# Kernel tuning notes

Hardware: AMD Instinct MI355X
Metric: run time of the kernel (lower is better)

Reference implementation:

```python
import jax, jax.numpy as jnp
import numpy as np

LS, BS, N_HID, N_PART, T, D_IN, M = 2, 16, 256, 512, 16, 64, 1
MID = N_PART // 2


def setup_inputs() -> dict:
    key = jax.random.key(0)
    ks = jax.random.split(key, 12)
    s = 0.1
    inp = {}
    inp["x"] = jax.random.normal(ks[0], (BS, T, D_IN), jnp.float32)
    inp["y"] = jax.random.normal(ks[1], (BS,), jnp.float32)
    inp["particles"] = jax.random.normal(ks[2], (LS, BS, N_HID, N_PART), jnp.float32)
    inp["weights"] = jnp.full((BS, N_PART), 1.0 / N_PART, jnp.float32)
    inp["q"] = jnp.asarray(1.0, jnp.float32)
    inp["e"] = jnp.asarray(0.1, jnp.float32)
    inp["r"] = jnp.asarray(0.5, jnp.float32)
    inp["Wih0"] = jax.random.normal(ks[3], (4 * N_HID, D_IN), jnp.float32) * s
    inp["Whh0"] = jax.random.normal(ks[4], (4 * N_HID, N_HID), jnp.float32) * s
    inp["b0"] = jnp.zeros((4 * N_HID,), jnp.float32)
    inp["Wih1"] = jax.random.normal(ks[5], (4 * N_HID, N_HID), jnp.float32) * s
    inp["Whh1"] = jax.random.normal(ks[6], (4 * N_HID, N_HID), jnp.float32) * s
    inp["b1"] = jnp.zeros((4 * N_HID,), jnp.float32)
    inp["Wh"] = jax.random.normal(ks[7], (M, N_HID), jnp.float32) * s
    inp["bh"] = jnp.zeros((M,), jnp.float32)
    inp["eps_h"] = jax.random.normal(ks[8], (MID, LS, BS, N_HID), jnp.float32)
    inp["eps_c"] = jax.random.normal(ks[9], (MID, LS, BS, N_HID), jnp.float32)
    u = jax.random.uniform(ks[10], (BS, 2, MID), jnp.float32, minval=1e-6, maxval=1.0)
    inp["gumbel"] = -jnp.log(-jnp.log(u))  # Gumbel noise for multinomial resampling
    return inp


def _lstm(x, h0, c0, Wih0, Whh0, b0, Wih1, Whh1, b1, q2, e2, eps_h, eps_c):
    # x: [bs,T,d]; h0,c0: [ls,bs,n]. Two-layer LSTM, noise added to final states.
    xs = jnp.swapaxes(x, 0, 1)  # [T,bs,d]

    def make_step(Wih, Whh, b):
        def step(carry, xt):
            h, c = carry
            g = xt @ Wih.T + h @ Whh.T + b
            i, f, gg, o = jnp.split(g, 4, axis=-1)
            c2 = jax.nn.sigmoid(f) * c + jax.nn.sigmoid(i) * jnp.tanh(gg)
            h2 = jax.nn.sigmoid(o) * jnp.tanh(c2)
            return (h2, c2), h2
        return step

    (hA, cA), out0 = jax.lax.scan(make_step(Wih0, Whh0, b0), (h0[0], c0[0]), xs)
    (hB, cB), out1 = jax.lax.scan(make_step(Wih1, Whh1, b1), (h0[1], c0[1]), out0)
    hT = jnp.stack([hA, hB]) + jnp.sqrt(q2) * eps_h
    cT = jnp.stack([cA, cB]) + jnp.sqrt(e2) * eps_c
    return jnp.swapaxes(out1, 0, 1), hT, cT


def _obs(u_last, Wh, bh):  # u_last: [bs,n,N] -> [bs,m,N]
    return jnp.einsum('mn,bnN->bmN', Wh, u_last) + bh[None, :, None]


def _estimate(Y, w, r):
    # Y: [bs,m,N], w: [bs,N]
    w_sum = jnp.sum(w, -1)
    W_mu = jnp.einsum('bmN,bN->bm', Y, w) / w_sum[:, None]
    cen = Y - W_mu[:, :, None]
    cov = jnp.einsum('bmN,bkN->bmk', cen, cen) / (Y.shape[-1] - 1)
    cov = cov + jnp.eye(Y.shape[1], dtype=Y.dtype) * (r * r)
    return W_mu, cov


def _inv_logdet(sig):
    m = sig.shape[-1]
    sig = sig + 1e-6 * jnp.eye(m, dtype=sig.dtype)
    L = jnp.linalg.cholesky(sig)
    inv_sig = jnp.linalg.inv(jnp.swapaxes(L, -2, -1)) @ jnp.linalg.inv(L)
    logdet = jnp.linalg.slogdet(sig)[1]
    return inv_sig, logdet


def reference(x, y, particles, weights, q, e, r, Wih0, Whh0, b0, Wih1, Whh1, b1, Wh, bh, eps_h, eps_c, gumbel):
    q2, e2 = q * q, e * e  # noise is squared before the transition (TransitionF)
    # ---- forecast_PF: particle i is h, particle i+MID is c ----
    h_parts = jnp.moveaxis(particles[..., :MID], -1, 0)  # [MID,ls,bs,n]
    c_parts = jnp.moveaxis(particles[..., MID:], -1, 0)
    step_fn = jax.vmap(lambda h0, c0, eh, ec: _lstm(x, h0, c0, Wih0, Whh0, b0, Wih1, Whh1, b1, q2, e2, eh, ec)[1:])
    hN, cN = step_fn(h_parts, c_parts, eps_h, eps_c)
    pr = jnp.moveaxis(jnp.concatenate([hN, cN], 0), 0, -1)  # [ls,bs,n,N]

    # ---- torch_PF weight update ----
    w = jnp.log(weights)
    Y = _obs(pr[-1], Wh, bh)  # [bs,m,N]
    W_mu_e, sig_e = _estimate(Y, w, r)  # NOTE: original passes LOG weights here (faithful)
    inv_sig, logdet = _inv_logdet(sig_e)
    w_sum = jnp.sum(w, -1)
    Wmu2 = Y * w[:, None, :] / w_sum[:, None, None]  # elementwise, as in w_likelihood
    innov = y[:, None, None] - Wmu2  # [bs,m,N]
    quad = jnp.einsum('bmN,bmk,bkN->bN', innov, inv_sig, innov)
    new_w = w + (-0.5 * logdet[:, None] - 0.5 * quad)
    # original: new_w -= log(sum(exp(new_w))) where python-sum reduces dim 0 -> [N]
    new_w = new_w - jnp.log(jnp.sum(jnp.exp(new_w), axis=0))[None, :]
    new_w = jnp.exp(new_w)

    # ---- per-batch, per-half soft resampling when neff < N/4 ----
    def resample_half(p, wh, g):  # p [ls,n,MID], wh [MID], g [MID]
        neff = 1.0 / jnp.sum(wh * wh)
        do = neff < (N_PART / 4.0)
        soft = 0.5 * wh + 0.5 / MID
        idx = jnp.argsort(-(jnp.log(soft) + g))  # weighted sample w/o replacement (Gumbel top-k)
        p_r = p[:, :, idx]
        lw = jnp.log(wh / soft)
        w_r = jnp.exp(lw - jax.nn.logsumexp(lw))
        return jnp.where(do, p_r, p), jnp.where(do, w_r, wh)

    def per_batch(p_b, w_b, g_b):  # p_b [ls,n,N], w_b [N], g_b [2,MID]
        p1, w1 = resample_half(p_b[:, :, :MID], w_b[:MID], g_b[0])
        p2, w2 = resample_half(p_b[:, :, MID:], w_b[MID:], g_b[1])
        return jnp.concatenate([p1, p2], -1), jnp.concatenate([w1, w2], 0)

    pf, wf = jax.vmap(per_batch, in_axes=(1, 0, 0), out_axes=(1, 0))(pr, new_w, gumbel)

    # ---- train=True branch: estimate / likelihood / NIS on filtered ensemble ----
    Yf = _obs(pf[-1], Wh, bh)
    W_mu, sig = _estimate(Yf, wf, r)
    inv_s, ld = _inv_logdet(sig)
    inn = y[:, None] - W_mu  # [bs,m]
    qf = jnp.einsum('bm,bmk,bk->b', inn, inv_s, inn)
    l = jnp.sum(-0.5 * ld - 0.5 * qf)
    nis = jnp.mean(qf)
    return W_mu, sig, pf, wf, l, nis
```

## Files before the change

### kernel.cpp

```cpp
#include <hip/hip_runtime.h>
#include <hip/hip_bf16.h>
#include <math.h>

#define LSN 2
#define BSN 16
#define NH 256
#define NP 512
#define MIDP 256
#define TTN 16
#define DIN 64
#define NCH 4096
#define GW 1024
#define PRS 268

typedef _Float16 f16;
typedef _Float16 f16x8 __attribute__((ext_vector_type(8)));
typedef float f32x4 __attribute__((ext_vector_type(4)));

__device__ __forceinline__ float fsig(float x){ return 1.0f/(1.0f+expf(-x)); }

__device__ __forceinline__ float brsum(float v, float* red){
  int tid = threadIdx.x;
  red[tid]=v; __syncthreads();
  for (int s=128; s>0; s>>=1){ if (tid<s) red[tid]+=red[tid+s]; __syncthreads(); }
  float r = red[0]; __syncthreads(); return r;
}

__device__ __forceinline__ int gsrow(int jp){
  return ((jp>>5)&3)*NH + (jp>>7)*32 + (jp&31);
}

__global__ void k_prep_w0(const float* __restrict__ Whh0, f16* __restrict__ W0i){
  int jp = blockIdx.x; int srow = gsrow(jp);
  W0i[(size_t)jp*NH + threadIdx.x] = (f16)Whh0[(size_t)srow*NH + threadIdx.x];
}
__global__ void k_prep_w1(const float* __restrict__ Wih1, const float* __restrict__ Whh1, f16* __restrict__ W1c){
  int jp = blockIdx.x; int srow = gsrow(jp);
  for (int p=0;p<2;++p){
    int k = p*256 + threadIdx.x;
    float v = (k < 256) ? Wih1[(size_t)srow*NH + k] : Whh1[(size_t)srow*NH + (k-256)];
    W1c[(size_t)jp*512 + k] = (f16)v;
  }
}
__global__ void k_prep_b1(const float* __restrict__ b1, float* __restrict__ b1i){
  int jp = blockIdx.x*256 + threadIdx.x;
  b1i[jp] = b1[gsrow(jp)];
}
__global__ void k_prep_xw0(const float* __restrict__ x, const float* __restrict__ Wih0,
                           const float* __restrict__ b0, float* __restrict__ xW0){
  int row = blockIdx.x;
  __shared__ float xr[DIN];
  if (threadIdx.x < DIN) xr[threadIdx.x] = x[(size_t)row*DIN + threadIdx.x];
  __syncthreads();
  int n = threadIdx.x;
  for (int q=0;q<4;++q){
    int wrow = q*NH + n;
    float acc = b0[wrow];
    #pragma unroll 8
    for (int d=0; d<DIN; ++d) acc += xr[d] * Wih0[(size_t)wrow*DIN + d];
    int jhat = (n>>5)*128 + q*32 + (n&31);
    xW0[(size_t)row*GW + jhat] = acc;
  }
}

__global__ __launch_bounds__(256) void k_init(const float* __restrict__ part,
                f16* __restrict__ h0, f16* __restrict__ h1,
                float* __restrict__ c0, float* __restrict__ c1){
  __shared__ float lh[64][65];
  __shared__ float lcv[64][65];
  int l = blockIdx.z, b = blockIdx.y;
  int i0 = (blockIdx.x >> 2)*64, n0 = (blockIdx.x & 3)*64;
  int tid = threadIdx.x;
  #pragma unroll
  for (int rep=0; rep<16; ++rep){
    int nn = rep*4 + (tid>>6);
    int ii = tid & 63;
    size_t rowb = ((size_t)(l*BSN + b)*NH + n0 + nn)*NP;
    lh[nn][ii]  = part[rowb + i0 + ii];
    lcv[nn][ii] = part[rowb + MIDP + i0 + ii];
  }
  __syncthreads();
  f16* h = l ? h1 : h0;
  float* c = l ? c1 : c0;
  #pragma unroll
  for (int rep=0; rep<16; ++rep){
    int ii = rep*4 + (tid>>6);
    int nn = tid & 63;
    size_t chain = (size_t)b*256 + i0 + ii;
    h[chain*NH + n0 + nn] = (f16)lh[nn][ii];
    c[chain*NH + n0 + nn] = lcv[nn][ii];
  }
}

struct StepCfg {
  const f16* A1; const f16* A2;
  float* C; f16* Hout;
  int layer; int t; int is_last;
};

__global__ __launch_bounds__(256) void k_step2(
    StepCfg cfgA, StepCfg cfgB,
    const f16* __restrict__ W0i, const f16* __restrict__ W1c,
    const float* __restrict__ xw0, const float* __restrict__ b1i,
    float* __restrict__ pr, const float* __restrict__ eps_h, const float* __restrict__ eps_c,
    const float* __restrict__ qp, const float* __restrict__ ep)
{
  __shared__ __align__(16) char smem[36864];
  f16* Asm = (f16*)smem;
  f16* Bsm = Asm + 128*72;

  const StepCfg cfg = blockIdx.z ? cfgB : cfgA;
  const int layer  = cfg.layer;
  const int Kt     = layer ? 512 : 256;
  const int nslice = layer ? 8 : 4;
  const f16* W     = layer ? W1c : W0i;

  const int tid = threadIdx.x;
  const int lane = tid & 63, wid = tid >> 6;
  const int lr = lane >> 4, lc = lane & 15;
  const int wm = wid * 32;
  const int m0 = blockIdx.x * 128;
  const int y  = blockIdx.y;
  const int bb = blockIdx.x >> 1;

  float cold[2][2][4];
  #pragma unroll
  for (int mi=0; mi<2; ++mi)
    #pragma unroll
    for (int mh=0; mh<2; ++mh)
      #pragma unroll
      for (int r=0; r<4; ++r)
        cold[mi][mh][r] = cfg.C[(size_t)(m0 + wm + mi*16 + lr*4 + r)*NH + y*32 + mh*16 + lc];

  f32x4 acc[2][8];
  #pragma unroll
  for (int mi=0;mi<2;++mi)
    #pragma unroll
    for (int ni=0;ni<8;++ni) acc[mi][ni] = (f32x4){0.f,0.f,0.f,0.f};

  const int srow = tid >> 1, sseg = (tid & 1)*32;
  for (int ks=0; ks<nslice; ++ks){
    __syncthreads();
    const f16* Ab; int ka;
    if (layer==1 && ks>=4){ Ab = cfg.A2; ka = (ks-4)*64; } else { Ab = cfg.A1; ka = ks*64; }
    {
      const float4* src = (const float4*)(Ab + (size_t)(m0+srow)*NH + ka + sseg);
      float4* dst = (float4*)(Asm + srow*72 + sseg);
      dst[0]=src[0]; dst[1]=src[1]; dst[2]=src[2]; dst[3]=src[3];
      const float4* srcB = (const float4*)(W + (size_t)(y*128+srow)*Kt + ks*64 + sseg);
      float4* dstB = (float4*)(Bsm + srow*72 + sseg);
      dstB[0]=srcB[0]; dstB[1]=srcB[1]; dstB[2]=srcB[2]; dstB[3]=srcB[3];
    }
    __syncthreads();
    #pragma unroll
    for (int k2=0;k2<2;++k2){
      const int koff = k2*32 + lr*8;
      f16x8 a0 = *(const f16x8*)(Asm + (wm +  0 + lc)*72 + koff);
      f16x8 a1 = *(const f16x8*)(Asm + (wm + 16 + lc)*72 + koff);
      f16x8 b[8];
      #pragma unroll
      for (int ni=0;ni<8;++ni) b[ni] = *(const f16x8*)(Bsm + (ni*16 + lc)*72 + koff);
      #pragma unroll
      for (int ni=0;ni<8;++ni){
        acc[0][ni] = __builtin_amdgcn_mfma_f32_16x16x32_f16(a0, b[ni], acc[0][ni], 0,0,0);
        acc[1][ni] = __builtin_amdgcn_mfma_f32_16x16x32_f16(a1, b[ni], acc[1][ni], 0,0,0);
      }
    }
  }

  float addv[4][2];
  {
    const float* ar = (layer==0) ? (xw0 + (size_t)(bb*TTN + cfg.t)*GW + y*128)
                                 : (b1i + y*128);
    #pragma unroll
    for (int q=0;q<4;++q)
      #pragma unroll
      for (int mh=0;mh<2;++mh)
        addv[q][mh] = ar[q*32 + mh*16 + lc];
  }

  float sq=0.f, se=0.f;
  float* prstage = (float*)smem;
  if (cfg.is_last){
    sq = sqrtf(qp[0]*qp[0]); se = sqrtf(ep[0]*ep[0]);
    __syncthreads();
  }

  #pragma unroll
  for (int mi=0;mi<2;++mi)
   #pragma unroll
   for (int mh=0;mh<2;++mh)
    #pragma unroll
    for (int r=0;r<4;++r){
      float gi = acc[mi][mh+0][r] + addv[0][mh];
      float gf = acc[mi][mh+2][r] + addv[1][mh];
      float gg = acc[mi][mh+4][r] + addv[2][mh];
      float go = acc[mi][mh+6][r] + addv[3][mh];
      float c2 = fsig(gf)*cold[mi][mh][r] + fsig(gi)*tanhf(gg);
      float h2 = fsig(go)*tanhf(c2);
      int ml = wm + mi*16 + lr*4 + r;
      int chain = m0 + ml;
      int nglob = y*32 + mh*16 + lc;
      cfg.Hout[(size_t)chain*NH + nglob] = (f16)h2;
      if (!cfg.is_last){
        cfg.C[(size_t)chain*NH + nglob] = c2;
      } else {
        int ip = (blockIdx.x & 1)*128 + ml;
        size_t eidx = ((size_t)(ip*LSN + layer)*BSN + bb)*NH + nglob;
        int nl = mh*16 + lc;
        prstage[nl*PRS + ml]       = h2 + sq*eps_h[eidx];
        prstage[nl*PRS + 128 + ml] = c2 + se*eps_c[eidx];
      }
    }

  if (cfg.is_last){
    __syncthreads();
    #pragma unroll
    for (int s=0;s<8;++s){
      int u = s*256 + tid;
      int nl = u >> 6, within = u & 63;
      int half = within >> 5, q4 = within & 31;
      size_t rowp = (size_t)(layer*BSN + bb)*NH + y*32 + nl;
      float4 v = *(const float4*)(prstage + nl*PRS + half*128 + q4*4);
      *(float4*)(pr + rowp*NP + half*MIDP + (blockIdx.x & 1)*128 + q4*4) = v;
    }
  }
}

__global__ void k_obs(const float* __restrict__ pr, const float* __restrict__ Wh,
                      const float* __restrict__ bh, float* __restrict__ Y){
  int b = blockIdx.x; int N = blockIdx.y*256 + threadIdx.x;
  float acc = bh[0];
  for (int n=0;n<NH;++n) acc += Wh[n] * pr[((size_t)(BSN + b)*NH + n)*NP + N];
  Y[(size_t)b*NP + N] = acc;
}

__global__ void k_stats1(const float* __restrict__ Y, const float* __restrict__ wts,
                         const float* __restrict__ yv, const float* __restrict__ rp,
                         float* __restrict__ pre){
  int b = blockIdx.x, tid = threadIdx.x;
  __shared__ float red[256];
  float lw0 = logf(wts[b*NP+tid]),     lw1 = logf(wts[b*NP+256+tid]);
  float y0  = Y[b*NP+tid],             y1  = Y[b*NP+256+tid];
  float SW = brsum(lw0+lw1, red);
  float SY = brsum(y0*lw0 + y1*lw1, red);
  float mu = SY/SW;
  float c0=y0-mu, c1=y1-mu;
  float SC = brsum(c0*c0+c1*c1, red);
  float sig = SC/511.0f + rp[0]*rp[0];
  float a = sig+1e-6f, inv = 1.0f/a, ld = logf(a);
  float yb = yv[b];
  float i0 = yb - y0*lw0/SW;
  float i1 = yb - y1*lw1/SW;
  pre[b*NP+tid]     = lw0 - 0.5f*ld - 0.5f*inv*i0*i0;
  pre[b*NP+256+tid] = lw1 - 0.5f*ld - 0.5f*inv*i1*i1;
}

__global__ void k_colsoftmax(const float* __restrict__ pre, float* __restrict__ neww){
  int N = blockIdx.x*256 + threadIdx.x;
  float s=0.f;
  for(int b=0;b<BSN;b++) s += expf(pre[b*NP+N]);
  float ls = logf(s);
  for(int b=0;b<BSN;b++) neww[b*NP+N] = expf(pre[b*NP+N] - ls);
}

__global__ void k_resample(const float* __restrict__ neww, const float* __restrict__ gum,
                           float* __restrict__ wf, int* __restrict__ idxb, int* __restrict__ dofl,
                           float* __restrict__ out){
  int b = blockIdx.x >> 1, hf = blockIdx.x & 1, j = threadIdx.x;
  __shared__ float red[256]; __shared__ float key[256];
  float wh = neww[b*NP + hf*256 + j];
  red[j] = wh*wh; __syncthreads();
  for (int s=128;s>0;s>>=1){ if(j<s) red[j]+=red[j+s]; __syncthreads(); }
  float s2 = red[0]; __syncthreads();
  int doit = (1.0f/s2) < (float)(NP)/4.0f;
  float soft = 0.5f*wh + (0.5f/(float)MIDP);
  float kk = logf(soft) + gum[(b*2+hf)*256 + j];
  key[j] = kk; __syncthreads();
  int rank = 0;
  for (int m=0;m<256;++m){ float km = key[m]; rank += (km > kk) || (km == kk && m < j); }
  idxb[(b*2+hf)*256 + rank] = j;
  float lw = logf(wh/soft);
  red[j] = lw; __syncthreads();
  for (int s=128;s>0;s>>=1){ if(j<s) red[j] = fmaxf(red[j],red[j+s]); __syncthreads(); }
  float mx = red[0]; __syncthreads();
  red[j] = expf(lw-mx); __syncthreads();
  for (int s=128;s>0;s>>=1){ if(j<s) red[j]+=red[j+s]; __syncthreads(); }
  float lse = mx + logf(red[0]);
  float wr = expf(lw - lse);
  float wv = doit ? wr : wh;
  wf[b*NP + hf*256 + j] = wv;
  out[4194336 + b*NP + hf*256 + j] = wv;
  if (j==0) dofl[b*2+hf] = doit;
}

__global__ void k_pfg(const float* __restrict__ pr, const int* __restrict__ idxb,
                      const int* __restrict__ dofl, float* __restrict__ out){
  size_t row = blockIdx.x;
  int b = (blockIdx.x >> 8) & 15;
  const float* src = pr + row*NP;
  for (int hf=0; hf<2; ++hf){
    int loc = threadIdx.x;
    int N = hf*256 + loc;
    int dcol = dofl[b*2+hf] ? hf*256 + idxb[(b*2+hf)*256 + loc] : N;
    out[32 + row*NP + N] = src[dcol];
  }
}

__global__ void k_yf(const float* __restrict__ Y, const int* __restrict__ idxb,
                     const int* __restrict__ dofl, float* __restrict__ Yf){
  int b = blockIdx.x; int N = threadIdx.x; int hf = N >> 8; int loc = N & 255;
  int dcol = dofl[b*2+hf] ? hf*256 + idxb[(b*2+hf)*256 + loc] : N;
  Yf[b*NP+N] = Y[b*NP+dcol];
}

__global__ void k_final_est(const float* __restrict__ Yf, const float* __restrict__ wf,
                            const float* __restrict__ yv, const float* __restrict__ rp,
                            float* __restrict__ qf, float* __restrict__ ldb,
                            float* __restrict__ out){
  int b = blockIdx.x, tid = threadIdx.x;
  __shared__ float red[256];
  float w0 = wf[b*NP+tid], w1 = wf[b*NP+256+tid];
  float y0 = Yf[b*NP+tid], y1 = Yf[b*NP+256+tid];
  float SW = brsum(w0+w1, red);
  float SY = brsum(y0*w0+y1*w1, red);
  float mu = SY/SW;
  float c0=y0-mu, c1=y1-mu;
  float SC = brsum(c0*c0+c1*c1, red);
  float sig = SC/511.0f + rp[0]*rp[0];
  if (tid==0){
    float a = sig + 1e-6f; float inv = 1.0f/a; float ld = logf(a);
    float inn = yv[b]-mu; float q = inn*inn*inv;
    qf[b]=q; ldb[b]=ld;
    out[b]      = mu;
    out[16 + b] = sig;
  }
}

__global__ void k_final_scalar(const float* __restrict__ qf, const float* __restrict__ ldb,
                               float* __restrict__ out){
  if (threadIdx.x==0){
    float l=0.f, nq=0.f;
    for(int b=0;b<BSN;b++){ l += -0.5f*ldb[b]-0.5f*qf[b]; nq += qf[b]; }
    out[4202528] = l;
    out[4202529] = nq/16.0f;
  }
}

extern "C" void kernel_launch(void* const* d_in, const int* in_sizes, int n_in,
                              void* d_out, int out_size, void* d_ws, size_t ws_size,
                              hipStream_t stream) {
  const float* x      = (const float*)d_in[0];
  const float* yv     = (const float*)d_in[1];
  const float* part   = (const float*)d_in[2];
  const float* wts    = (const float*)d_in[3];
  const float* qp     = (const float*)d_in[4];
  const float* ep     = (const float*)d_in[5];
  const float* rp     = (const float*)d_in[6];
  const float* Wih0   = (const float*)d_in[7];
  const float* Whh0   = (const float*)d_in[8];
  const float* b0     = (const float*)d_in[9];
  const float* Wih1   = (const float*)d_in[10];
  const float* Whh1   = (const float*)d_in[11];
  const float* b1     = (const float*)d_in[12];
  const float* Wh     = (const float*)d_in[13];
  const float* bh     = (const float*)d_in[14];
  const float* eps_h  = (const float*)d_in[15];
  const float* eps_c  = (const float*)d_in[16];
  const float* gum    = (const float*)d_in[17];
  float* out = (float*)d_out;

  char* p = (char*)d_ws;
  f16*   W0i  = (f16*)p;  p += (size_t)GW*NH*2;
  f16*   W1c  = (f16*)p;  p += (size_t)GW*512*2;
  float* b1i  = (float*)p; p += (size_t)GW*4;
  float* xW0  = (float*)p; p += (size_t)256*GW*4;
  f16*   h0A  = (f16*)p;  p += (size_t)NCH*NH*2;
  f16*   h0B  = (f16*)p;  p += (size_t)NCH*NH*2;
  f16*   h1A  = (f16*)p;  p += (size_t)NCH*NH*2;
  f16*   h1B  = (f16*)p;  p += (size_t)NCH*NH*2;
  float* c0   = (float*)p; p += (size_t)NCH*NH*4;
  float* c1   = (float*)p; p += (size_t)NCH*NH*4;
  float* pr   = (float*)p; p += (size_t)LSN*BSN*NH*NP*4;
  float* Yb   = (float*)p; p += 32768;
  float* pre  = (float*)p; p += 32768;
  float* neww = (float*)p; p += 32768;
  float* wf   = (float*)p; p += 32768;
  float* Yf   = (float*)p; p += 32768;
  int*   idxb = (int*)p;   p += 32768;
  int*   dofl = (int*)p;   p += 128;
  float* qf   = (float*)p; p += 64;
  float* ldb  = (float*)p; p += 64;

  k_prep_w0 <<<1024, 256, 0, stream>>>(Whh0, W0i);
  k_prep_w1 <<<1024, 256, 0, stream>>>(Wih1, Whh1, W1c);
  k_prep_b1 <<<4, 256, 0, stream>>>(b1, b1i);
  k_prep_xw0<<<256, 256, 0, stream>>>(x, Wih0, b0, xW0);
  k_init    <<<dim3(16,16,2), 256, 0, stream>>>(part, h0A, h1A, c0, c1);

  {
    StepCfg s0{h0A, nullptr, c0, h0B, 0, 0, 0};
    k_step2<<<dim3(32,8,1), 256, 0, stream>>>(s0, s0, W0i, W1c, xW0, b1i,
        pr, eps_h, eps_c, qp, ep);
  }
  f16 *h0cur=h0B, *h0nxt=h0A, *h1cur=h1A, *h1nxt=h1B;
  for (int t=0; t<15; ++t){
    StepCfg ca{h0cur, nullptr, c0, h0nxt, 0, t+1, (t+1==15) ? 1 : 0};
    StepCfg cb{h0cur, h1cur,   c1, h1nxt, 1, t,   0};
    k_step2<<<dim3(32,8,2), 256, 0, stream>>>(ca, cb, W0i, W1c, xW0, b1i,
        pr, eps_h, eps_c, qp, ep);
    f16* tmp = h0cur; h0cur = h0nxt; h0nxt = tmp;
    tmp = h1cur; h1cur = h1nxt; h1nxt = tmp;
  }
  {
    StepCfg fin{h0cur, h1cur, c1, h1nxt, 1, 15, 1};
    k_step2<<<dim3(32,8,1), 256, 0, stream>>>(fin, fin, W0i, W1c, xW0, b1i,
        pr, eps_h, eps_c, qp, ep);
  }

  k_obs       <<<dim3(16,2), 256, 0, stream>>>(pr, Wh, bh, Yb);
  k_stats1    <<<16, 256, 0, stream>>>(Yb, wts, yv, rp, pre);
  k_colsoftmax<<<2, 256, 0, stream>>>(pre, neww);
  k_resample  <<<32, 256, 0, stream>>>(neww, gum, wf, idxb, dofl, out);
  k_pfg       <<<8192, 256, 0, stream>>>(pr, idxb, dofl, out);
  k_yf        <<<16, 512, 0, stream>>>(Yb, idxb, dofl, Yf);
  k_final_est <<<16, 256, 0, stream>>>(Yf, wf, yv, rp, qf, ldb, out);
  k_final_scalar<<<1, 64, 0, stream>>>(qf, ldb, out);
}
```

Baseline: 432.6 us.

## Double-buffer LSTM step tiles, fuse prep/obs/stats/yf kernels, coarsen gather

The LSTM step kernel now prefetches the next K-slice into registers while the MFMAs run on the current slice. It uses two LDS buffers, so only one barrier is needed per slice. The three weight-prep kernels are merged into one, the observation and stats kernels are fused into a single 512-thread block per batch, and the Yf gather moves into the resample kernel. The particle gather kernel now runs 128 blocks, each copying 64 rows with a shared column map. Doubling LDS lowers possible occupancy, and the much smaller gather grid may underuse memory bandwidth.

```diff
diff --git a/kernel.cpp b/kernel.cpp
--- a/kernel.cpp
+++ b/kernel.cpp
@@ -12,6 +12,7 @@
 #define NCH 4096
 #define GW 1024
 #define PRS 268
+#define BUFSZ 36864
 
 typedef _Float16 f16;
 typedef _Float16 f16x8 __attribute__((ext_vector_type(8)));
@@ -19,6 +20,12 @@
 
 __device__ __forceinline__ float fsig(float x){ return 1.0f/(1.0f+expf(-x)); }
 
+__device__ __forceinline__ float brsum512(float v, float* red){
+  int tid = threadIdx.x;
+  red[tid]=v; __syncthreads();
+  for (int s=256; s>0; s>>=1){ if (tid<s) red[tid]+=red[tid+s]; __syncthreads(); }
+  float r = red[0]; __syncthreads(); return r;
+}
 __device__ __forceinline__ float brsum(float v, float* red){
   int tid = threadIdx.x;
   red[tid]=v; __syncthreads();
@@ -30,21 +37,14 @@
   return ((jp>>5)&3)*NH + (jp>>7)*32 + (jp&31);
 }
 
-__global__ void k_prep_w0(const float* __restrict__ Whh0, f16* __restrict__ W0i){
-  int jp = blockIdx.x; int srow = gsrow(jp);
-  W0i[(size_t)jp*NH + threadIdx.x] = (f16)Whh0[(size_t)srow*NH + threadIdx.x];
-}
-__global__ void k_prep_w1(const float* __restrict__ Wih1, const float* __restrict__ Whh1, f16* __restrict__ W1c){
-  int jp = blockIdx.x; int srow = gsrow(jp);
-  for (int p=0;p<2;++p){
-    int k = p*256 + threadIdx.x;
-    float v = (k < 256) ? Wih1[(size_t)srow*NH + k] : Whh1[(size_t)srow*NH + (k-256)];
-    W1c[(size_t)jp*512 + k] = (f16)v;
-  }
-}
-__global__ void k_prep_b1(const float* __restrict__ b1, float* __restrict__ b1i){
-  int jp = blockIdx.x*256 + threadIdx.x;
-  b1i[jp] = b1[gsrow(jp)];
+__global__ void k_prep_w(const float* __restrict__ Whh0, const float* __restrict__ Wih1,
+                         const float* __restrict__ Whh1, const float* __restrict__ b1,
+                         f16* __restrict__ W0i, f16* __restrict__ W1c, float* __restrict__ b1i){
+  int jp = blockIdx.x; int srow = gsrow(jp); int t = threadIdx.x;
+  W0i[(size_t)jp*NH + t]        = (f16)Whh0[(size_t)srow*NH + t];
+  W1c[(size_t)jp*512 + t]       = (f16)Wih1[(size_t)srow*NH + t];
+  W1c[(size_t)jp*512 + 256 + t] = (f16)Whh1[(size_t)srow*NH + t];
+  if (t==0) b1i[jp] = b1[srow];
 }
 __global__ void k_prep_xw0(const float* __restrict__ x, const float* __restrict__ Wih0,
                            const float* __restrict__ b0, float* __restrict__ xW0){
@@ -105,9 +105,7 @@
     float* __restrict__ pr, const float* __restrict__ eps_h, const float* __restrict__ eps_c,
     const float* __restrict__ qp, const float* __restrict__ ep)
 {
-  __shared__ __align__(16) char smem[36864];
-  f16* Asm = (f16*)smem;
-  f16* Bsm = Asm + 128*72;
+  __shared__ __align__(16) char smem[2*BUFSZ];
 
   const StepCfg cfg = blockIdx.z ? cfgB : cfgA;
   const int layer  = cfg.layer;
@@ -139,33 +137,49 @@
     for (int ni=0;ni<8;++ni) acc[mi][ni] = (f32x4){0.f,0.f,0.f,0.f};
 
   const int srow = tid >> 1, sseg = (tid & 1)*32;
-  for (int ks=0; ks<nslice; ++ks){
-    __syncthreads();
+
+  float4 ra0,ra1,ra2,ra3, rb0,rb1,rb2,rb3;
+  auto loadslice = [&](int ks){
     const f16* Ab; int ka;
     if (layer==1 && ks>=4){ Ab = cfg.A2; ka = (ks-4)*64; } else { Ab = cfg.A1; ka = ks*64; }
-    {
-      const float4* src = (const float4*)(Ab + (size_t)(m0+srow)*NH + ka + sseg);
-      float4* dst = (float4*)(Asm + srow*72 + sseg);
-      dst[0]=src[0]; dst[1]=src[1]; dst[2]=src[2]; dst[3]=src[3];
-      const float4* srcB = (const float4*)(W + (size_t)(y*128+srow)*Kt + ks*64 + sseg);
-      float4* dstB = (float4*)(Bsm + srow*72 + sseg);
-      dstB[0]=srcB[0]; dstB[1]=srcB[1]; dstB[2]=srcB[2]; dstB[3]=srcB[3];
-    }
-    __syncthreads();
+    const float4* sa = (const float4*)(Ab + (size_t)(m0+srow)*NH + ka + sseg);
+    const float4* sb = (const float4*)(W + (size_t)(y*128+srow)*Kt + (size_t)ks*64 + sseg);
+    ra0=sa[0]; ra1=sa[1]; ra2=sa[2]; ra3=sa[3];
+    rb0=sb[0]; rb1=sb[1]; rb2=sb[2]; rb3=sb[3];
+  };
+  auto writeslice = [&](int buf){
+    f16* base = (f16*)(smem + buf*BUFSZ);
+    float4* da = (float4*)(base + srow*72 + sseg);
+    da[0]=ra0; da[1]=ra1; da[2]=ra2; da[3]=ra3;
+    float4* db = (float4*)(base + 128*72 + srow*72 + sseg);
+    db[0]=rb0; db[1]=rb1; db[2]=rb2; db[3]=rb3;
+  };
+
+  loadslice(0);
+  writeslice(0);
+  __syncthreads();
+  for (int ks=0; ks<nslice; ++ks){
+    const int cur = ks & 1;
+    const bool more = (ks+1) < nslice;
+    if (more) loadslice(ks+1);
+    const f16* bufA = (const f16*)(smem + cur*BUFSZ);
+    const f16* bufB = bufA + 128*72;
     #pragma unroll
     for (int k2=0;k2<2;++k2){
       const int koff = k2*32 + lr*8;
-      f16x8 a0 = *(const f16x8*)(Asm + (wm +  0 + lc)*72 + koff);
-      f16x8 a1 = *(const f16x8*)(Asm + (wm + 16 + lc)*72 + koff);
+      f16x8 a0 = *(const f16x8*)(bufA + (wm +  0 + lc)*72 + koff);
+      f16x8 a1 = *(const f16x8*)(bufA + (wm + 16 + lc)*72 + koff);
       f16x8 b[8];
       #pragma unroll
-      for (int ni=0;ni<8;++ni) b[ni] = *(const f16x8*)(Bsm + (ni*16 + lc)*72 + koff);
+      for (int ni=0;ni<8;++ni) b[ni] = *(const f16x8*)(bufB + (ni*16 + lc)*72 + koff);
       #pragma unroll
       for (int ni=0;ni<8;++ni){
         acc[0][ni] = __builtin_amdgcn_mfma_f32_16x16x32_f16(a0, b[ni], acc[0][ni], 0,0,0);
         acc[1][ni] = __builtin_amdgcn_mfma_f32_16x16x32_f16(a1, b[ni], acc[1][ni], 0,0,0);
       }
     }
+    if (more) writeslice(cur ^ 1);
+    __syncthreads();
   }
 
   float addv[4][2];
@@ -183,7 +197,6 @@
   float* prstage = (float*)smem;
   if (cfg.is_last){
     sq = sqrtf(qp[0]*qp[0]); se = sqrtf(ep[0]*ep[0]);
-    __syncthreads();
   }
 
   #pragma unroll
@@ -227,33 +240,25 @@
   }
 }
 
-__global__ void k_obs(const float* __restrict__ pr, const float* __restrict__ Wh,
-                      const float* __restrict__ bh, float* __restrict__ Y){
-  int b = blockIdx.x; int N = blockIdx.y*256 + threadIdx.x;
+__global__ void k_obs_stats(const float* __restrict__ pr, const float* __restrict__ Wh,
+                            const float* __restrict__ bh, const float* __restrict__ wts,
+                            const float* __restrict__ yv, const float* __restrict__ rp,
+                            float* __restrict__ Y, float* __restrict__ pre){
+  int b = blockIdx.x; int N = threadIdx.x;
+  __shared__ float red[512];
   float acc = bh[0];
   for (int n=0;n<NH;++n) acc += Wh[n] * pr[((size_t)(BSN + b)*NH + n)*NP + N];
   Y[(size_t)b*NP + N] = acc;
-}
-
-__global__ void k_stats1(const float* __restrict__ Y, const float* __restrict__ wts,
-                         const float* __restrict__ yv, const float* __restrict__ rp,
-                         float* __restrict__ pre){
-  int b = blockIdx.x, tid = threadIdx.x;
-  __shared__ float red[256];
-  float lw0 = logf(wts[b*NP+tid]),     lw1 = logf(wts[b*NP+256+tid]);
-  float y0  = Y[b*NP+tid],             y1  = Y[b*NP+256+tid];
-  float SW = brsum(lw0+lw1, red);
-  float SY = brsum(y0*lw0 + y1*lw1, red);
+  float lw = logf(wts[b*NP+N]);
+  float SW = brsum512(lw, red);
+  float SY = brsum512(acc*lw, red);
   float mu = SY/SW;
-  float c0=y0-mu, c1=y1-mu;
-  float SC = brsum(c0*c0+c1*c1, red);
+  float cen = acc-mu;
+  float SC = brsum512(cen*cen, red);
   float sig = SC/511.0f + rp[0]*rp[0];
   float a = sig+1e-6f, inv = 1.0f/a, ld = logf(a);
-  float yb = yv[b];
-  float i0 = yb - y0*lw0/SW;
-  float i1 = yb - y1*lw1/SW;
-  pre[b*NP+tid]     = lw0 - 0.5f*ld - 0.5f*inv*i0*i0;
-  pre[b*NP+256+tid] = lw1 - 0.5f*ld - 0.5f*inv*i1*i1;
+  float i0 = yv[b] - acc*lw/SW;
+  pre[b*NP+N] = lw - 0.5f*ld - 0.5f*inv*i0*i0;
 }
 
 __global__ void k_colsoftmax(const float* __restrict__ pre, float* __restrict__ neww){
@@ -265,10 +270,11 @@
 }
 
 __global__ void k_resample(const float* __restrict__ neww, const float* __restrict__ gum,
+                           const float* __restrict__ Y,
                            float* __restrict__ wf, int* __restrict__ idxb, int* __restrict__ dofl,
-                           float* __restrict__ out){
+                           float* __restrict__ Yf, float* __restrict__ out){
   int b = blockIdx.x >> 1, hf = blockIdx.x & 1, j = threadIdx.x;
-  __shared__ float red[256]; __shared__ float key[256];
+  __shared__ float red[256]; __shared__ float key[256]; __shared__ int sidx[256];
   float wh = neww[b*NP + hf*256 + j];
   red[j] = wh*wh; __syncthreads();
   for (int s=128;s>0;s>>=1){ if(j<s) red[j]+=red[j+s]; __syncthreads(); }
@@ -279,7 +285,11 @@
   key[j] = kk; __syncthreads();
   int rank = 0;
   for (int m=0;m<256;++m){ float km = key[m]; rank += (km > kk) || (km == kk && m < j); }
-  idxb[(b*2+hf)*256 + rank] = j;
+  sidx[rank] = j; __syncthreads();
+  idxb[(b*2+hf)*256 + j] = sidx[j];
+  int N = hf*256 + j;
+  int dcol = doit ? hf*256 + sidx[j] : N;
+  Yf[b*NP + N] = Y[b*NP + dcol];
   float lw = logf(wh/soft);
   red[j] = lw; __syncthreads();
   for (int s=128;s>0;s>>=1){ if(j<s) red[j] = fmaxf(red[j],red[j+s]); __syncthreads(); }
@@ -289,29 +299,33 @@
   float lse = mx + logf(red[0]);
   float wr = expf(lw - lse);
   float wv = doit ? wr : wh;
-  wf[b*NP + hf*256 + j] = wv;
-  out[4194336 + b*NP + hf*256 + j] = wv;
+  wf[b*NP + N] = wv;
+  out[4194336 + b*NP + N] = wv;
   if (j==0) dofl[b*2+hf] = doit;
 }
 
 __global__ void k_pfg(const float* __restrict__ pr, const int* __restrict__ idxb,
                       const int* __restrict__ dofl, float* __restrict__ out){
-  size_t row = blockIdx.x;
-  int b = (blockIdx.x >> 8) & 15;
-  const float* src = pr + row*NP;
+  __shared__ int dcol[512];
+  int blk = blockIdx.x;
+  int q = blk & 3, lb = blk >> 2;
+  int b = lb & 15;
+  int tid = threadIdx.x;
+  #pragma unroll
   for (int hf=0; hf<2; ++hf){
-    int loc = threadIdx.x;
-    int N = hf*256 + loc;
-    int dcol = dofl[b*2+hf] ? hf*256 + idxb[(b*2+hf)*256 + loc] : N;
-    out[32 + row*NP + N] = src[dcol];
-  }
-}
-
-__global__ void k_yf(const float* __restrict__ Y, const int* __restrict__ idxb,
-                     const int* __restrict__ dofl, float* __restrict__ Yf){
-  int b = blockIdx.x; int N = threadIdx.x; int hf = N >> 8; int loc = N & 255;
-  int dcol = dofl[b*2+hf] ? hf*256 + idxb[(b*2+hf)*256 + loc] : N;
-  Yf[b*NP+N] = Y[b*NP+dcol];
+    int N = hf*256 + tid;
+    dcol[N] = dofl[b*2+hf] ? hf*256 + idxb[(b*2+hf)*256 + tid] : N;
+  }
+  __syncthreads();
+  int d0 = dcol[tid], d1 = dcol[tid+256];
+  size_t rowbase = (size_t)lb*NH + q*64;
+  for (int rr=0; rr<64; ++rr){
+    size_t row = rowbase + rr;
+    const float* src = pr + row*NP;
+    float* dst = out + 32 + row*NP;
+    dst[tid]     = src[d0];
+    dst[tid+256] = src[d1];
+  }
 }
 
 __global__ void k_final_est(const float* __restrict__ Yf, const float* __restrict__ wf,
@@ -392,9 +406,7 @@
   float* qf   = (float*)p; p += 64;
   float* ldb  = (float*)p; p += 64;
 
-  k_prep_w0 <<<1024, 256, 0, stream>>>(Whh0, W0i);
-  k_prep_w1 <<<1024, 256, 0, stream>>>(Wih1, Whh1, W1c);
-  k_prep_b1 <<<4, 256, 0, stream>>>(b1, b1i);
+  k_prep_w  <<<1024, 256, 0, stream>>>(Whh0, Wih1, Whh1, b1, W0i, W1c, b1i);
   k_prep_xw0<<<256, 256, 0, stream>>>(x, Wih0, b0, xW0);
   k_init    <<<dim3(16,16,2), 256, 0, stream>>>(part, h0A, h1A, c0, c1);
 
@@ -418,12 +430,10 @@
         pr, eps_h, eps_c, qp, ep);
   }
 
-  k_obs       <<<dim3(16,2), 256, 0, stream>>>(pr, Wh, bh, Yb);
-  k_stats1    <<<16, 256, 0, stream>>>(Yb, wts, yv, rp, pre);
+  k_obs_stats <<<16, 512, 0, stream>>>(pr, Wh, bh, wts, yv, rp, Yb, pre);
   k_colsoftmax<<<2, 256, 0, stream>>>(pre, neww);
-  k_resample  <<<32, 256, 0, stream>>>(neww, gum, wf, idxb, dofl, out);
-  k_pfg       <<<8192, 256, 0, stream>>>(pr, idxb, dofl, out);
-  k_yf        <<<16, 512, 0, stream>>>(Yb, idxb, dofl, Yf);
+  k_resample  <<<32, 256, 0, stream>>>(neww, gum, Yb, wf, idxb, dofl, Yf, out);
+  k_pfg       <<<128, 256, 0, stream>>>(pr, idxb, dofl, out);
   k_final_est <<<16, 256, 0, stream>>>(Yf, wf, yv, rp, qf, ldb, out);
   k_final_scalar<<<1, 64, 0, stream>>>(qf, ldb, out);
 }
```

New measurement: 400.7 us. -7.4%, faster.
